# Performance work log

Measured on AMD Instinct MI355X. Metric: run time of the kernel, lower is better.

The kernel has to match this reference:

```python
import jax, jax.numpy as jnp
import numpy as np

NINP, NHID, NTOK, NLAYERS, BSZ = 4096, 512, 50257, 2, 32
T_ENC, T_DEC = 80, 40


def lstm_layer(x, h0, c0, Wih, Whh, b):
    """Single LSTM layer over a [T,B,in] sequence; PyTorch gate order i,f,g,o."""
    def step(carry, xt):
        h, c = carry
        z = xt @ Wih.T + h @ Whh.T + b  # [B, 4H]
        i, f, g, o = jnp.split(z, 4, axis=-1)
        c = jax.nn.sigmoid(f) * c + jax.nn.sigmoid(i) * jnp.tanh(g)
        h = jax.nn.sigmoid(o) * jnp.tanh(c)
        return (h, c), h
    (hN, cN), ys = jax.lax.scan(step, (h0, c0), x)
    return ys, hN, cN


def multi_lstm(x, h0, c0, params):
    """Stacked LSTM; params = list of (Wih, Whh, b) per layer."""
    hs, cs = [], []
    y = x
    for l, (Wih, Whh, b) in enumerate(params):
        y, hN, cN = lstm_layer(y, h0[l], c0[l], Wih, Whh, b)
        hs.append(hN); cs.append(cN)
    return y, jnp.stack(hs), jnp.stack(cs)


def setup_inputs():
    key = jax.random.key(0)
    ks = iter(jax.random.split(key, 32))
    def rn(shape, scale=0.05):
        return (jax.random.normal(next(ks), shape, dtype=jnp.float32) * scale)
    H4 = 4 * NHID
    d = {}
    d["inp"] = rn((T_ENC, BSZ, NINP), 1.0)
    for name in ("hid1_h", "hid1_c", "hid2_h", "hid2_c"):
        d[name] = jnp.zeros((NLAYERS, BSZ, NHID), jnp.float32)
    # lstm1: layer0 in=NINP, layer1 in=NHID (b = b_ih + b_hh fused)
    d["l1_Wih0"] = rn((H4, NINP)); d["l1_Whh0"] = rn((H4, NHID)); d["l1_b0"] = rn((H4,))
    d["l1_Wih1"] = rn((H4, NHID)); d["l1_Whh1"] = rn((H4, NHID)); d["l1_b1"] = rn((H4,))
    # lstm2: layer0 in=2*NHID, layer1 in=NHID
    d["l2_Wih0"] = rn((H4, 2 * NHID)); d["l2_Whh0"] = rn((H4, NHID)); d["l2_b0"] = rn((H4,))
    d["l2_Wih1"] = rn((H4, NHID)); d["l2_Whh1"] = rn((H4, NHID)); d["l2_b1"] = rn((H4,))
    d["W_out"] = rn((NTOK, NHID)); d["b_out"] = rn((NTOK,))
    d["W_emb"] = rn((NHID, NTOK)); d["b_emb"] = rn((NHID,))
    d["target_len"] = T_DEC
    return d


def reference(inp, hid1_h, hid1_c, hid2_h, hid2_c,
              l1_Wih0, l1_Whh0, l1_b0, l1_Wih1, l1_Whh1, l1_b1,
              l2_Wih0, l2_Whh0, l2_b0, l2_Wih1, l2_Whh1, l2_b1,
              W_out, b_out, W_emb, b_emb, target_len):
    p1 = [(l1_Wih0, l1_Whh0, l1_b0), (l1_Wih1, l1_Whh1, l1_b1)]
    p2 = [(l2_Wih0, l2_Whh0, l2_b0), (l2_Wih1, l2_Whh1, l2_b1)]
    T, B, ninp = inp.shape
    H = hid1_h.shape[-1]
    # --- encoding stage ---
    out1, h1, c1 = multi_lstm(inp, hid1_h, hid1_c, p1)
    pad_h = jnp.zeros((T, B, H), inp.dtype)
    _, h2, c2 = multi_lstm(jnp.concatenate([pad_h, out1], axis=-1), hid2_h, hid2_c, p2)
    # --- decoding stage ---
    pad_in = jnp.zeros((target_len, B, ninp), inp.dtype)
    out1d, _, _ = multi_lstm(pad_in, h1, c1, p1)
    # vocab2emb(one-hot BOS at index 0) = W_emb[:, 0] + b_emb; never updated in
    # the original loop (variable-name bug), so it is constant over decode steps,
    # making the per-step loop equivalent to one lstm2 scan.
    bos_emb = W_emb[:, 0] + b_emb  # [H]
    bos = jnp.broadcast_to(bos_emb, (target_len, B, H))
    out2d, _, _ = multi_lstm(jnp.concatenate([bos, out1d], axis=-1), h2, c2, p2)
    logits = jnp.einsum('tbh,vh->tbv', out2d, W_out) + b_out  # [T_dec, B, V]
    return jax.nn.log_softmax(logits, axis=-1)
```

## Files before the change

### kernel.cpp

```cpp
#include <hip/hip_runtime.h>
#include <hip/hip_bf16.h>
#include <cstddef>

#define NINP 4096
#define NHID 512
#define G4   2048
#define NTOK 50257
#define BSZ  32
#define T_ENC 80
#define T_DEC 40

typedef __attribute__((ext_vector_type(4))) float  f32x4;
typedef __attribute__((ext_vector_type(4))) __bf16 bf16x4;
typedef __attribute__((ext_vector_type(8))) __bf16 bf16x8;

__device__ __forceinline__ int sw_off(int r, int k) {
    return r * 128 + ((((k >> 3) ^ (r & 7)) << 4) | ((k & 7) << 1));
}
__device__ __forceinline__ int sw512(int r, int k) {
    return r * 1024 + ((((k >> 3) ^ (r & 7)) << 4) | ((k & 7) << 1));
}

__device__ __forceinline__ bf16x4 hi4(const float4& v) {
    bf16x4 h; h[0] = (__bf16)v.x; h[1] = (__bf16)v.y;
    h[2] = (__bf16)v.z; h[3] = (__bf16)v.w; return h;
}

__device__ __forceinline__ void split8(const float4& a, const float4& b,
                                       bf16x8& h, bf16x8& l) {
    float x[8] = {a.x, a.y, a.z, a.w, b.x, b.y, b.z, b.w};
    #pragma unroll
    for (int i = 0; i < 8; i++) {
        __bf16 hb = (__bf16)x[i];
        h[i] = hb; l[i] = (__bf16)(x[i] - (float)hb);
    }
}

__device__ __forceinline__ bf16x8 to_bf16x8(const float4& a, const float4& b) {
    bf16x8 r;
    r[0]=(__bf16)a.x; r[1]=(__bf16)a.y; r[2]=(__bf16)a.z; r[3]=(__bf16)a.w;
    r[4]=(__bf16)b.x; r[5]=(__bf16)b.y; r[6]=(__bf16)b.z; r[7]=(__bf16)b.w;
    return r;
}

__device__ __forceinline__ void unpack8(const uint4& a, const uint4& b,
                                        bf16x8& h, bf16x8& l) {
    unsigned u[8] = {a.x, a.y, a.z, a.w, b.x, b.y, b.z, b.w};
    union { unsigned short s; __bf16 v; } t;
    #pragma unroll
    for (int i = 0; i < 8; i++) {
        t.s = (unsigned short)(u[i] & 0xffff); h[i] = t.v;
        t.s = (unsigned short)(u[i] >> 16);    l[i] = t.v;
    }
}
__device__ __forceinline__ bf16x8 unpack_hi8(const uint4& a, const uint4& b) {
    unsigned u[8] = {a.x, a.y, a.z, a.w, b.x, b.y, b.z, b.w};
    union { unsigned short s; __bf16 v; } t;
    bf16x8 h;
    #pragma unroll
    for (int i = 0; i < 8; i++) { t.s = (unsigned short)(u[i] & 0xffff); h[i] = t.v; }
    return h;
}

__device__ __forceinline__ unsigned pack_hilo(float x) {
    __bf16 hb = (__bf16)x;
    float hf = (float)hb;
    __bf16 lb = (__bf16)(x - hf);
    union { __bf16 b; unsigned short s; } ch, cl;
    ch.b = hb; cl.b = lb;
    return (unsigned)ch.s | ((unsigned)cl.s << 16);
}

__device__ __forceinline__ float fast_sigmoid(float x) {
    return 1.f / (1.f + __expf(-x));
}
__device__ __forceinline__ float fast_tanh(float x) {
    return 1.f - 2.f / (__expf(2.f * x) + 1.f);
}

__global__ __launch_bounds__(256) void gemm_ahi(
    const float* __restrict__ A, int lda,
    const float* __restrict__ B, int ldb,
    const float* __restrict__ bias,
    float* __restrict__ Z, int ldz,
    int N, int K)
{
    __shared__ __align__(16) char lds[32768];
    const int tid  = threadIdx.x;
    const int bm   = blockIdx.y * 128;
    const int bn   = blockIdx.x * 128;
    const int wave = tid >> 6;
    const int lane = tid & 63;
    const int wm   = (wave >> 1) * 64;
    const int wn   = (wave & 1) * 64;
    const int lr   = lane & 15;
    const int kg   = lane >> 4;

    const int rr = tid >> 4;
    const int kk = (tid & 15) * 4;

    f32x4 acc[4][4] = {};

    for (int k0 = 0; k0 < K; k0 += 64) {
        float4 av[8], bv[8];
        #pragma unroll
        for (int i = 0; i < 8; i++) {
            int r = i * 16 + rr;
            av[i] = *(const float4*)&A[(size_t)(bm + r) * lda + k0 + kk];
            int rb = bn + r;
            if (rb < N)
                bv[i] = *(const float4*)&B[(size_t)rb * ldb + k0 + kk];
            else
                bv[i] = make_float4(0.f, 0.f, 0.f, 0.f);
        }
        __syncthreads();
        #pragma unroll
        for (int i = 0; i < 8; i++) {
            int r = i * 16 + rr;
            int off = sw_off(r, kk);
            *(bf16x4*)(lds + off)         = hi4(av[i]);
            *(bf16x4*)(lds + 16384 + off) = hi4(bv[i]);
        }
        __syncthreads();
        #pragma unroll
        for (int ks = 0; ks < 2; ks++) {
            bf16x8 ah[4], bh[4];
            const int kbase = ks * 32 + kg * 8;
            #pragma unroll
            for (int f = 0; f < 4; f++) {
                ah[f] = *(const bf16x8*)(lds + sw_off(wm + f * 16 + lr, kbase));
                bh[f] = *(const bf16x8*)(lds + 16384 + sw_off(wn + f * 16 + lr, kbase));
            }
            #pragma unroll
            for (int fm = 0; fm < 4; fm++)
                #pragma unroll
                for (int fn = 0; fn < 4; fn++)
                    acc[fm][fn] = __builtin_amdgcn_mfma_f32_16x16x32_bf16(
                        ah[fm], bh[fn], acc[fm][fn], 0, 0, 0);
        }
        __syncthreads();
    }

    #pragma unroll
    for (int fn = 0; fn < 4; fn++) {
        int col = bn + wn + fn * 16 + lr;
        if (col < N) {
            float bb = bias ? bias[col] : 0.f;
            #pragma unroll
            for (int fm = 0; fm < 4; fm++) {
                #pragma unroll
                for (int j = 0; j < 4; j++) {
                    int row = bm + wm + fm * 16 + kg * 4 + j;
                    Z[(size_t)row * ldz + col] = acc[fm][fn][j] + bb;
                }
            }
        }
    }
}

__global__ __launch_bounds__(256, 2) void gemm_vocab64(
    const __bf16* __restrict__ Ah,
    const float* __restrict__ B,
    const float* __restrict__ bias,
    float* __restrict__ Z)
{
    __shared__ __align__(16) char lds[81920];
    char* ldsB = lds;
    char* ldsA = lds + 65536;

    const int tid  = threadIdx.x;
    const int bn   = blockIdx.x * 64;
    const int wave = tid >> 6;
    const int lane = tid & 63;
    const int wm   = (wave >> 1) * 64;
    const int wn   = (wave & 1) * 32;
    const int lr   = lane & 15;
    const int kg   = lane >> 4;

    #pragma unroll 4
    for (int jj = 0; jj < 16; jj++) {
        int e = tid + jj * 256;
        int row = e >> 6;
        int k = (e & 63) * 8;
        int gr = bn + row;
        float4 v0, v1;
        if (gr < NTOK) {
            v0 = *(const float4*)&B[(size_t)gr * 512 + k];
            v1 = *(const float4*)&B[(size_t)gr * 512 + k + 4];
        } else {
            v0 = make_float4(0.f,0.f,0.f,0.f); v1 = v0;
        }
        *(bf16x8*)(ldsB + sw512(row, k)) = to_bf16x8(v0, v1);
    }

    float bb[2];
    #pragma unroll
    for (int fn = 0; fn < 2; fn++) {
        int col = bn + wn + fn * 16 + lr;
        bb[fn] = (col < NTOK) ? bias[col] : 0.f;
    }
    __syncthreads();

    for (int mt = 0; mt < 10; mt++) {
        f32x4 acc[4][2] = {};
        for (int k0 = 0; k0 < 8; k0++) {
            __syncthreads();
            #pragma unroll
            for (int jj = 0; jj < 4; jj++) {
                int e = tid + jj * 256;
                int row = e >> 3;
                int k = (e & 7) * 8;
                uint4 v = *(const uint4*)&Ah[(size_t)(mt * 128 + row) * 512 + k0 * 64 + k];
                *(uint4*)(ldsA + sw_off(row, k)) = v;
            }
            __syncthreads();
            #pragma unroll
            for (int ks = 0; ks < 2; ks++) {
                bf16x8 ah[4], bh[2];
                const int ka = ks * 32 + kg * 8;
                #pragma unroll
                for (int f = 0; f < 4; f++)
                    ah[f] = *(const bf16x8*)(ldsA + sw_off(wm + f * 16 + lr, ka));
                #pragma unroll
                for (int f = 0; f < 2; f++)
                    bh[f] = *(const bf16x8*)(ldsB + sw512(wn + f * 16 + lr, k0 * 64 + ka));
                #pragma unroll
                for (int fm = 0; fm < 4; fm++)
                    #pragma unroll
                    for (int fn = 0; fn < 2; fn++)
                        acc[fm][fn] = __builtin_amdgcn_mfma_f32_16x16x32_bf16(
                            ah[fm], bh[fn], acc[fm][fn], 0, 0, 0);
            }
        }
        #pragma unroll
        for (int fn = 0; fn < 2; fn++) {
            int col = bn + wn + fn * 16 + lr;
            if (col < NTOK) {
                #pragma unroll
                for (int fm = 0; fm < 4; fm++) {
                    #pragma unroll
                    for (int j = 0; j < 4; j++) {
                        int row = mt * 128 + wm + fm * 16 + kg * 4 + j;
                        Z[(size_t)row * NTOK + col] = acc[fm][fn][j] + bb[fn];
                    }
                }
            }
        }
    }
}

__device__ __forceinline__ void grid_barrier(unsigned* flags, unsigned* gen,
                                             unsigned target)
{
    __syncthreads();
    if (threadIdx.x == 0) {
        __builtin_amdgcn_fence(__ATOMIC_RELEASE, "agent");
        __hip_atomic_store(&flags[blockIdx.x], target, __ATOMIC_RELAXED,
                           __HIP_MEMORY_SCOPE_AGENT);
    }
    if (blockIdx.x == 0) {
        while (__hip_atomic_load(&flags[threadIdx.x], __ATOMIC_RELAXED,
                                 __HIP_MEMORY_SCOPE_AGENT) < target)
            ;
        __syncthreads();
        if (threadIdx.x == 0)
            __hip_atomic_store(gen, target, __ATOMIC_RELAXED,
                               __HIP_MEMORY_SCOPE_AGENT);
    }
    if (threadIdx.x == 0) {
        while (__hip_atomic_load(gen, __ATOMIC_RELAXED,
                                 __HIP_MEMORY_SCOPE_AGENT) < target)
            __builtin_amdgcn_s_sleep(1);
        __builtin_amdgcn_fence(__ATOMIC_ACQUIRE, "agent");
    }
    __syncthreads();
}

__global__ __launch_bounds__(256, 1) void fused_scan(
    const float* __restrict__ Zx,
    const float* __restrict__ Whh_0, const float* __restrict__ bias_0,
    const float* __restrict__ Wih_1, const float* __restrict__ Whh_1,
    const float* __restrict__ bias_1,
    const float* __restrict__ Wih_2, const float* __restrict__ Whh_2,
    const float* __restrict__ bias_2e, const float* __restrict__ bias_2d,
    const float* __restrict__ Wih_3, const float* __restrict__ Whh_3,
    const float* __restrict__ bias_3,
    const float* __restrict__ hid1_h, const float* __restrict__ hid1_c,
    const float* __restrict__ hid2_h, const float* __restrict__ hid2_c,
    __bf16* __restrict__ dec3h,
    unsigned* hbuf, unsigned* flags, unsigned* gen)
{
    __shared__ __align__(16) char lds[131072];
    float* a_x = (float*)(lds + 32768);

    const int tid  = threadIdx.x;
    const int L    = blockIdx.x >> 6;
    const int bidc = blockIdx.x & 63;
    const int wave = tid >> 6;
    const int lane = tid & 63;
    const int mh   = wave >> 1;
    const int nh   = wave & 1;
    const int lr   = lane & 15;
    const int kg   = lane >> 4;
    const int jcbase = bidc * 8;
    const int bq = tid >> 3;
    const int aq = tid & 7;

    const float* Whh = (L==0)?Whh_0:(L==1)?Whh_1:(L==2)?Whh_2:Whh_3;
    const float* Wih = (L==1)?Wih_1:(L==2)?Wih_2:(L==3)?Wih_3:nullptr;
    const int ld_ih  = (L==2)?1024:512;
    const float* be  = (L==0)?bias_0:(L==1)?bias_1:(L==2)?bias_2e:bias_3;
    const float* bd  = (L==2)?bias_2d:be;
    const float* h0  = ((L<2)?hid1_h:hid2_h) + (L&1)*16384;
    const float* c0  = ((L<2)?hid1_c:hid2_c) + (L&1)*16384;
    unsigned* myb       = hbuf + L*32768;
    const unsigned* xsb = hbuf + (L>0 ? (L-1)*32768 : 0);

    {
        int gate = (bq<8)?0:(bq<16)?2:(bq<24)?1:3;
        int row  = gate*512 + jcbase + (bq&7);
        const float* wr = Whh + (size_t)row * 512;
        #pragma unroll
        for (int jj = 0; jj < 8; jj++) {
            int k = aq*8 + jj*64;
            *(bf16x8*)(lds + 65536 + sw512(bq, k)) =
                to_bf16x8(*(const float4*)(wr+k), *(const float4*)(wr+k+4));
        }
        if (Wih) {
            const float* wr2 = Wih + (size_t)row * ld_ih;
            #pragma unroll
            for (int jj = 0; jj < 8; jj++) {
                int k = aq*8 + jj*64;
                *(bf16x8*)(lds + 98304 + sw512(bq, k)) =
                    to_bf16x8(*(const float4*)(wr2+k), *(const float4*)(wr2+k+4));
            }
        }
    }

    const int n_col = nh*16 + lr;
    const int gate  = (n_col<8)?0:(n_col<16)?2:(n_col<24)?1:3;
    const int col2048 = gate*512 + jcbase + (n_col & 7);
    const float bbe = be[col2048];
    const float bbd = bd[col2048];

    float cc[4] = {0.f, 0.f, 0.f, 0.f};
    if (nh == 1 && lr < 8) {
        #pragma unroll
        for (int j = 0; j < 4; j++)
            cc[j] = c0[(mh*16 + kg*4 + j)*512 + jcbase + lr];
    }

    float zxr[4] = {0.f, 0.f, 0.f, 0.f};
    if (L == 0) {
        #pragma unroll
        for (int j = 0; j < 4; j++)
            zxr[j] = Zx[(size_t)(mh*16 + kg*4 + j)*G4 + col2048];
    }
    __syncthreads();

    const int rowA = mh*16 + lr;
    const int rowB = nh*16 + lr;

    for (int tt = 0; tt < 123; ++tt) {
        const int myt = tt - L;
        if (myt >= 0 && myt < 120) {
            uint4 xr[8][2];
            if (L > 0) {
                const unsigned* xs = xsb + (size_t)(myt & 1)*16384 + bq*512;
                #pragma unroll
                for (int jj = 0; jj < 8; jj++) {
                    int k = aq*8 + jj*64;
                    xr[jj][0] = *(const uint4*)(xs + k);
                    xr[jj][1] = *(const uint4*)(xs + k + 4);
                }
            }
            if (myt == 0) {
                const float* hr = h0 + bq*512;
                #pragma unroll
                for (int jj = 0; jj < 8; jj++) {
                    int k = aq*8 + jj*64;
                    bf16x8 H, Lo;
                    split8(*(const float4*)(hr+k), *(const float4*)(hr+k+4), H, Lo);
                    int off = sw512(bq, k);
                    *(bf16x8*)(lds + off)         = H;
                    *(bf16x8*)(lds + 32768 + off) = Lo;
                }
            } else {
                const unsigned* hs = myb + (size_t)((myt-1) & 1)*16384 + bq*512;
                #pragma unroll
                for (int jj = 0; jj < 8; jj++) {
                    int k = aq*8 + jj*64;
                    bf16x8 H, Lo;
                    unpack8(*(const uint4*)(hs+k), *(const uint4*)(hs+k+4), H, Lo);
                    int off = sw512(bq, k);
                    *(bf16x8*)(lds + off)         = H;
                    *(bf16x8*)(lds + 32768 + off) = Lo;
                }
            }
            __syncthreads();

            f32x4 accA = {0.f,0.f,0.f,0.f}, accB = {0.f,0.f,0.f,0.f};
            #pragma unroll
            for (int ks = 0; ks < 16; ++ks) {
                int k = ks*32 + kg*8;
                int offA = sw512(rowA, k);
                int offB = sw512(rowB, k);
                bf16x8 ah = *(const bf16x8*)(lds + offA);
                bf16x8 al = *(const bf16x8*)(lds + 32768 + offA);
                bf16x8 bh = *(const bf16x8*)(lds + 65536 + offB);
                accA = __builtin_amdgcn_mfma_f32_16x16x32_bf16(ah, bh, accA, 0,0,0);
                accB = __builtin_amdgcn_mfma_f32_16x16x32_bf16(al, bh, accB, 0,0,0);
            }
            __syncthreads();

            if (L > 0) {
                #pragma unroll
                for (int jj = 0; jj < 8; jj++) {
                    int k = aq*8 + jj*64;
                    *(bf16x8*)(lds + sw512(bq, k)) = unpack_hi8(xr[jj][0], xr[jj][1]);
                }
                __syncthreads();
                #pragma unroll
                for (int ks = 0; ks < 16; ++ks) {
                    int k = ks*32 + kg*8;
                    bf16x8 ax = *(const bf16x8*)(lds + sw512(rowA, k));
                    bf16x8 bi = *(const bf16x8*)(lds + 98304 + sw512(rowB, k));
                    accA = __builtin_amdgcn_mfma_f32_16x16x32_bf16(ax, bi, accA, 0,0,0);
                }
            }

            const float bbv = (L == 2 && myt >= 80) ? bbd : bbe;
            float z[4];
            #pragma unroll
            for (int j = 0; j < 4; j++)
                z[j] = accA[j] + accB[j] + bbv
                     + ((L == 0 && myt < 80) ? zxr[j] : 0.f);

            {
                int mytn = myt + 1;
                if (L == 0 && mytn < 80) {
                    #pragma unroll
                    for (int j = 0; j < 4; j++)
                        zxr[j] = Zx[(size_t)mytn*(BSZ*G4)
                                    + (mh*16+kg*4+j)*G4 + col2048];
                }
            }

            if (nh == 0) {
                float zo[4];
                #pragma unroll
                for (int j = 0; j < 4; j++) zo[j] = __shfl_xor(z[j], 8);
                if (lr < 8) {
                    #pragma unroll
                    for (int j = 0; j < 4; j++)
                        a_x[(mh*16 + kg*4 + j)*8 + lr] =
                            fast_sigmoid(z[j]) * fast_tanh(zo[j]);
                }
            }
            __syncthreads();

            if (nh == 1) {
                float cnew[4] = {0.f,0.f,0.f,0.f};
                if (lr < 8) {
                    #pragma unroll
                    for (int j = 0; j < 4; j++) {
                        float av = a_x[(mh*16 + kg*4 + j)*8 + lr];
                        cnew[j] = fast_sigmoid(z[j]) * cc[j] + av;
                        cc[j] = cnew[j];
                    }
                }
                float cfrom[4];
                #pragma unroll
                for (int j = 0; j < 4; j++) cfrom[j] = __shfl_xor(cnew[j], 8);
                if (lr >= 8) {
                    #pragma unroll
                    for (int j = 0; j < 4; j++) {
                        float hn = fast_sigmoid(z[j]) * fast_tanh(cfrom[j]);
                        int b = mh*16 + kg*4 + j;
                        int hcol = jcbase + (lr - 8);
                        if (L == 3 && myt >= 80)
                            dec3h[(size_t)(myt-80)*(BSZ*NHID) + b*512 + hcol] =
                                (__bf16)hn;
                        __hip_atomic_store(&myb[(size_t)(myt & 1)*16384 + b*512 + hcol],
                                           pack_hilo(hn), __ATOMIC_RELAXED,
                                           __HIP_MEMORY_SCOPE_AGENT);
                    }
                }
            }
        }
        grid_barrier(flags, gen, (unsigned)tt + 1u);
    }
}

__global__ __launch_bounds__(256) void bias2_kernel(
    const float* __restrict__ W_emb,
    const float* __restrict__ b_emb,
    const float* __restrict__ Wih0,
    const float* __restrict__ b0,
    float* __restrict__ bias2)
{
    __shared__ float bos[NHID];
    const int tid = threadIdx.x;
    for (int i = tid; i < NHID; i += 256)
        bos[i] = W_emb[(size_t)i * NTOK] + b_emb[i];
    __syncthreads();
    int j = blockIdx.x * 256 + tid;
    float acc = b0[j];
    for (int k = 0; k < NHID; k++)
        acc += bos[k] * Wih0[(size_t)j * 1024 + k];
    bias2[j] = acc;
}

__global__ __launch_bounds__(256) void logsoftmax_kernel(float* __restrict__ logits)
{
    const size_t row = blockIdx.x;
    float* p = logits + row * (size_t)NTOK;
    const int tid = threadIdx.x;

    const int head = (int)((4 - (((size_t)row * NTOK) & 3)) & 3);
    const int nv   = (NTOK - head) >> 2;
    const int tail = head + nv * 4;
    float4* p4 = (float4*)(p + head);

    float m = -1e30f, s = 0.f;
    auto upd = [&](float x) {
        if (x <= m) {
            s += __expf(x - m);
        } else {
            s = s * __expf(m - x) + 1.f;
            m = x;
        }
    };

    for (int i = tid; i < head; i += 256) upd(p[i]);
    for (int i = tid; i < nv; i += 256) {
        float4 v = p4[i];
        upd(v.x); upd(v.y); upd(v.z); upd(v.w);
    }
    for (int i = tail + tid; i < NTOK; i += 256) upd(p[i]);

    #pragma unroll
    for (int off = 32; off > 0; off >>= 1) {
        float mo = __shfl_down(m, off);
        float so = __shfl_down(s, off);
        float mn = fmaxf(m, mo);
        s = s * __expf(m - mn) + so * __expf(mo - mn);
        m = mn;
    }
    __shared__ float sm[4], ss[4];
    if ((tid & 63) == 0) { sm[tid >> 6] = m; ss[tid >> 6] = s; }
    __syncthreads();
    float M4 = fmaxf(fmaxf(sm[0], sm[1]), fmaxf(sm[2], sm[3]));
    float S  = ss[0] * __expf(sm[0] - M4) + ss[1] * __expf(sm[1] - M4)
             + ss[2] * __expf(sm[2] - M4) + ss[3] * __expf(sm[3] - M4);
    float lse = M4 + logf(S);

    for (int i = tid; i < head; i += 256) p[i] -= lse;
    for (int i = tid; i < nv; i += 256) {
        float4 v = p4[i];
        v.x -= lse; v.y -= lse; v.z -= lse; v.w -= lse;
        p4[i] = v;
    }
    for (int i = tail + tid; i < NTOK; i += 256) p[i] -= lse;
}

extern "C" void kernel_launch(void* const* d_in, const int* in_sizes, int n_in,
                              void* d_out, int out_size, void* d_ws, size_t ws_size,
                              hipStream_t stream)
{
    const float* inp     = (const float*)d_in[0];
    const float* hid1_h  = (const float*)d_in[1];
    const float* hid1_c  = (const float*)d_in[2];
    const float* hid2_h  = (const float*)d_in[3];
    const float* hid2_c  = (const float*)d_in[4];
    const float* l1_Wih0 = (const float*)d_in[5];
    const float* l1_Whh0 = (const float*)d_in[6];
    const float* l1_b0   = (const float*)d_in[7];
    const float* l1_Wih1 = (const float*)d_in[8];
    const float* l1_Whh1 = (const float*)d_in[9];
    const float* l1_b1   = (const float*)d_in[10];
    const float* l2_Wih0 = (const float*)d_in[11];
    const float* l2_Whh0 = (const float*)d_in[12];
    const float* l2_b0   = (const float*)d_in[13];
    const float* l2_Wih1 = (const float*)d_in[14];
    const float* l2_Whh1 = (const float*)d_in[15];
    const float* l2_b1   = (const float*)d_in[16];
    const float* W_out   = (const float*)d_in[17];
    const float* b_out   = (const float*)d_in[18];
    const float* W_emb   = (const float*)d_in[19];
    const float* b_emb   = (const float*)d_in[20];

    float* out = (float*)d_out;
    float* ws  = (float*)d_ws;

    float* Zx    = ws;
    float* bias2 = ws + 5242880;
    __bf16* dec3h = (__bf16*)(ws + 5244928);
    unsigned* hbuf  = (unsigned*)(ws + 5572608);
    unsigned* flags = (unsigned*)(ws + 5703680);
    unsigned* gen   = flags + 256;

    (void)hipMemsetAsync(flags, 0, 1028, stream);

    {
        dim3 grid((G4 + 127) / 128, (T_ENC * BSZ) / 128);
        gemm_ahi<<<grid, dim3(256), 0, stream>>>(
            inp, NINP, l1_Wih0, NINP, nullptr, Zx, G4, G4, NINP);
    }
    bias2_kernel<<<8, 256, 0, stream>>>(W_emb, b_emb, l2_Wih0, l2_b0, bias2);

    fused_scan<<<256, 256, 0, stream>>>(
        Zx,
        l1_Whh0, l1_b0,
        l1_Wih1, l1_Whh1, l1_b1,
        l2_Wih0 + 512, l2_Whh0, l2_b0, bias2,
        l2_Wih1, l2_Whh1, l2_b1,
        hid1_h, hid1_c, hid2_h, hid2_c,
        dec3h, hbuf, flags, gen);

    gemm_vocab64<<<(NTOK + 63) / 64, dim3(256), 0, stream>>>(
        dec3h, W_out, b_out, out);
    logsoftmax_kernel<<<1280, dim3(256), 0, stream>>>(out);
}
```

Before: 1.815 ms.

## Fuse softmax exp-sum into vocab GEMM epilogue, split logsoftmax into lse+subtract

The vocab GEMM epilogue now computes per-row partial sums of exp(logit) for each 64-column panel, reduces them across lanes and waves, and writes them to a partials buffer. A small kernel sums the 786 partials per row and takes the log, and a final kernel subtracts the lse. This removes the separate read pass over the full logits matrix that the old logsoftmax did for max and sum. It drops max subtraction, so exp can overflow if logits are large. It also adds an exp per output element in the GEMM and a serial 786-step sum per row.

New measurement: 1.871 ms. 3.1% more time.

```diff
diff --git a/kernel.cpp b/kernel.cpp
--- a/kernel.cpp
+++ b/kernel.cpp
@@ -9,6 +9,7 @@
 #define BSZ  32
 #define T_ENC 80
 #define T_DEC 40
+#define NPAN 786
 
 typedef __attribute__((ext_vector_type(4))) float  f32x4;
 typedef __attribute__((ext_vector_type(4))) __bf16 bf16x4;
@@ -162,14 +163,16 @@
     const __bf16* __restrict__ Ah,
     const float* __restrict__ B,
     const float* __restrict__ bias,
-    float* __restrict__ Z)
+    float* __restrict__ Z,
+    float* __restrict__ part)
 {
     __shared__ __align__(16) char lds[81920];
     char* ldsB = lds;
     char* ldsA = lds + 65536;
 
     const int tid  = threadIdx.x;
-    const int bn   = blockIdx.x * 64;
+    const int bnp  = blockIdx.x;
+    const int bn   = bnp * 64;
     const int wave = tid >> 6;
     const int lane = tid & 63;
     const int wm   = (wave >> 1) * 64;
@@ -232,21 +235,79 @@
                             ah[fm], bh[fn], acc[fm][fn], 0, 0, 0);
             }
         }
+        float pex[4][4] = {};
         #pragma unroll
         for (int fn = 0; fn < 2; fn++) {
             int col = bn + wn + fn * 16 + lr;
-            if (col < NTOK) {
-                #pragma unroll
-                for (int fm = 0; fm < 4; fm++) {
-                    #pragma unroll
-                    for (int j = 0; j < 4; j++) {
+            bool valid = col < NTOK;
+            #pragma unroll
+            for (int fm = 0; fm < 4; fm++) {
+                #pragma unroll
+                for (int j = 0; j < 4; j++) {
+                    float zv = acc[fm][fn][j] + bb[fn];
+                    if (valid) {
                         int row = mt * 128 + wm + fm * 16 + kg * 4 + j;
-                        Z[(size_t)row * NTOK + col] = acc[fm][fn][j] + bb[fn];
+                        Z[(size_t)row * NTOK + col] = zv;
+                        pex[fm][j] += __expf(zv);
                     }
                 }
             }
         }
-    }
+        #pragma unroll
+        for (int off = 1; off < 16; off <<= 1)
+            #pragma unroll
+            for (int fm = 0; fm < 4; fm++)
+                #pragma unroll
+                for (int j = 0; j < 4; j++)
+                    pex[fm][j] += __shfl_xor(pex[fm][j], off);
+
+        __syncthreads();
+        float* rowpart = (float*)ldsA;
+        if (lr == 0) {
+            #pragma unroll
+            for (int fm = 0; fm < 4; fm++)
+                #pragma unroll
+                for (int j = 0; j < 4; j++)
+                    rowpart[(wm + fm * 16 + kg * 4 + j) * 2 + (wave & 1)] =
+                        pex[fm][j];
+        }
+        __syncthreads();
+        if (tid < 128)
+            part[(size_t)bnp * 1280 + mt * 128 + tid] =
+                rowpart[tid * 2] + rowpart[tid * 2 + 1];
+    }
+}
+
+__global__ __launch_bounds__(64) void lse_kernel(
+    const float* __restrict__ part, float* __restrict__ lse)
+{
+    int row = blockIdx.x * 64 + threadIdx.x;
+    float s = 0.f;
+    for (int p = 0; p < NPAN; p++)
+        s += part[(size_t)p * 1280 + row];
+    lse[row] = logf(s);
+}
+
+__global__ __launch_bounds__(256) void subtract_kernel(
+    float* __restrict__ logits, const float* __restrict__ lse)
+{
+    const size_t row = blockIdx.x;
+    float* p = logits + row * (size_t)NTOK;
+    const float l = lse[row];
+    const int tid = threadIdx.x;
+
+    const int head = (int)((4 - (((size_t)row * NTOK) & 3)) & 3);
+    const int nv   = (NTOK - head) >> 2;
+    const int tail = head + nv * 4;
+    float4* p4 = (float4*)(p + head);
+
+    for (int i = tid; i < head; i += 256) p[i] -= l;
+    for (int i = tid; i < nv; i += 256) {
+        float4 v = p4[i];
+        v.x -= l; v.y -= l; v.z -= l; v.w -= l;
+        p4[i] = v;
+    }
+    for (int i = tail + tid; i < NTOK; i += 256) p[i] -= l;
 }
 
 __device__ __forceinline__ void grid_barrier(unsigned* flags, unsigned* gen,
@@ -509,59 +570,6 @@
     for (int k = 0; k < NHID; k++)
         acc += bos[k] * Wih0[(size_t)j * 1024 + k];
     bias2[j] = acc;
-}
-
-__global__ __launch_bounds__(256) void logsoftmax_kernel(float* __restrict__ logits)
-{
-    const size_t row = blockIdx.x;
-    float* p = logits + row * (size_t)NTOK;
-    const int tid = threadIdx.x;
-
-    const int head = (int)((4 - (((size_t)row * NTOK) & 3)) & 3);
-    const int nv   = (NTOK - head) >> 2;
-    const int tail = head + nv * 4;
-    float4* p4 = (float4*)(p + head);
-
-    float m = -1e30f, s = 0.f;
-    auto upd = [&](float x) {
-        if (x <= m) {
-            s += __expf(x - m);
-        } else {
-            s = s * __expf(m - x) + 1.f;
-            m = x;
-        }
-    };
-
-    for (int i = tid; i < head; i += 256) upd(p[i]);
-    for (int i = tid; i < nv; i += 256) {
-        float4 v = p4[i];
-        upd(v.x); upd(v.y); upd(v.z); upd(v.w);
-    }
-    for (int i = tail + tid; i < NTOK; i += 256) upd(p[i]);
-
-    #pragma unroll
-    for (int off = 32; off > 0; off >>= 1) {
-        float mo = __shfl_down(m, off);
-        float so = __shfl_down(s, off);
-        float mn = fmaxf(m, mo);
-        s = s * __expf(m - mn) + so * __expf(mo - mn);
-        m = mn;
-    }
-    __shared__ float sm[4], ss[4];
-    if ((tid & 63) == 0) { sm[tid >> 6] = m; ss[tid >> 6] = s; }
-    __syncthreads();
-    float M4 = fmaxf(fmaxf(sm[0], sm[1]), fmaxf(sm[2], sm[3]));
-    float S  = ss[0] * __expf(sm[0] - M4) + ss[1] * __expf(sm[1] - M4)
-             + ss[2] * __expf(sm[2] - M4) + ss[3] * __expf(sm[3] - M4);
-    float lse = M4 + logf(S);
-
-    for (int i = tid; i < head; i += 256) p[i] -= lse;
-    for (int i = tid; i < nv; i += 256) {
-        float4 v = p4[i];
-        v.x -= lse; v.y -= lse; v.z -= lse; v.w -= lse;
-        p4[i] = v;
-    }
-    for (int i = tail + tid; i < NTOK; i += 256) p[i] -= lse;
 }
 
 extern "C" void kernel_launch(void* const* d_in, const int* in_sizes, int n_in,
@@ -599,6 +607,8 @@
     unsigned* hbuf  = (unsigned*)(ws + 5572608);
     unsigned* flags = (unsigned*)(ws + 5703680);
     unsigned* gen   = flags + 256;
+    float* part = ws + 5710848;
+    float* lse  = part + (size_t)NPAN * 1280;
 
     (void)hipMemsetAsync(flags, 0, 1028, stream);
 
@@ -618,7 +628,8 @@
         hid1_h, hid1_c, hid2_h, hid2_c,
         dec3h, hbuf, flags, gen);
 
-    gemm_vocab64<<<(NTOK + 63) / 64, dim3(256), 0, stream>>>(
-        dec3h, W_out, b_out, out);
-    logsoftmax_kernel<<<1280, dim3(256), 0, stream>>>(out);
-}
+    gemm_vocab64<<<NPAN, dim3(256), 0, stream>>>(
+        dec3h, W_out, b_out, out, part);
+    lse_kernel<<<20, dim3(64), 0, stream>>>(part, lse);
+    subtract_kernel<<<1280, dim3(256), 0, stream>>>(out, lse);
+}
```
